# Performance work log

Measured on AMD Instinct MI355X. Metric: run time of the kernel, lower is better.

## Reference

```python
import jax, jax.numpy as jnp
import numpy as np

N = 50000
E = 1600000
IN_DIM = 128
H = 8
D = 16  # out_dim per head


def setup_inputs() -> dict:
    key = jax.random.key(0)
    ks = jax.random.split(key, 9)
    h = jax.random.normal(ks[0], (N, IN_DIM), dtype=jnp.float32)
    src = jax.random.randint(ks[1], (E,), 0, N, dtype=jnp.int32)
    dst = jax.random.randint(ks[2], (E,), 0, N, dtype=jnp.int32)
    s = 1.0 / np.sqrt(IN_DIM)
    WQ = jax.random.uniform(ks[3], (IN_DIM, H * D), jnp.float32, -s, s)
    WK = jax.random.uniform(ks[4], (IN_DIM, H * D), jnp.float32, -s, s)
    WV = jax.random.uniform(ks[5], (IN_DIM, H * D), jnp.float32, -s, s)
    bQ = jax.random.uniform(ks[6], (H * D,), jnp.float32, -s, s)
    bK = jax.random.uniform(ks[7], (H * D,), jnp.float32, -s, s)
    bV = jax.random.uniform(ks[8], (H * D,), jnp.float32, -s, s)
    return {"h": h, "src": src, "dst": dst, "WQ": WQ, "WK": WK, "WV": WV,
            "bQ": bQ, "bK": bK, "bV": bV}


def reference(h, src, dst, WQ, WK, WV, bQ, bK, bV):
    # Node projections -> [N, H, D]
    Q = (h @ WQ + bQ).reshape(-1, H, D)
    K = (h @ WK + bK).reshape(-1, H, D)
    V = (h @ WV + bV).reshape(-1, H, D)
    # Edge scores: dot(K[src], Q[dst]) per head, scaled+clamped exp -> [E, H]
    scale = jnp.float32(np.sqrt(D))
    score = jnp.exp(jnp.clip(jnp.sum(K[src] * Q[dst], axis=-1) / scale, -5.0, 5.0))
    # Scatter-sum to destination nodes
    wV = jax.ops.segment_sum(score[:, :, None] * V[src], dst, num_segments=N)  # [N, H, D]
    z = jax.ops.segment_sum(score, dst, num_segments=N)  # [N, H]
    return wV / z[:, :, None]
```

## Files before the change

kernel.cpp:

```cpp
#include <hip/hip_runtime.h>

#define N_NODES 50000
#define N_PAD   50048
#define N_EDGES 1600000
#define HD 128
#define CHUNK 4096
#define NCHUNK ((N_EDGES + CHUNK - 1) / CHUNK)
#define NBUCKET ((N_NODES + 127) / 128)
#define PROJ_BLOCKS (N_PAD / 64)

typedef __attribute__((ext_vector_type(8))) short short8;
typedef __attribute__((ext_vector_type(4))) float floatx4;
typedef __attribute__((ext_vector_type(2))) float float2v;

union U4S8 { uint4 u; short8 s; };

__device__ __forceinline__ unsigned short f2bf(float f) {
    unsigned u = __float_as_uint(f);
    unsigned r = (u + 0x7fffu + ((u >> 16) & 1u)) >> 16;
    return (unsigned short)r;
}

__global__ __launch_bounds__(256) void k_chunkhist(
    const int* __restrict__ dst, int* __restrict__ chunkhist, int* __restrict__ btot,
    const float* __restrict__ WQ, const float* __restrict__ WK, const float* __restrict__ WV,
    unsigned short* __restrict__ Wf) {
    int t = threadIdx.x, c = blockIdx.x;
    if (c >= NCHUNK) {
        int tid = (c - NCHUNK) * 256 + t;
        int lane = tid & 63;
        int kstep = (tid >> 6) & 3;
        int ntile = tid >> 8;
        int g = ntile >> 3;
        int col = (ntile & 7) * 16 + (lane & 15);
        int k0 = kstep * 32 + (lane >> 4) * 8;
        const float* W = (g == 0) ? WQ : (g == 1) ? WK : WV;
        unsigned short r[8];
#pragma unroll
        for (int j = 0; j < 8; ++j)
            r[j] = f2bf(W[(size_t)(k0 + j) * HD + col]);
        *(uint4*)(Wf + (size_t)tid * 8) = *(uint4*)r;
        return;
    }
    __shared__ int hist[NBUCKET];
    for (int i = t; i < NBUCKET; i += 256) hist[i] = 0;
    __syncthreads();
    int e0 = c * CHUNK;
    int cnt = min(CHUNK, N_EDGES - e0);
    const uint4* d4 = (const uint4*)(dst + e0);
    int cnt4 = cnt >> 2;
    for (int i = t; i < cnt4; i += 256) {
        uint4 v = d4[i];
        atomicAdd(&hist[v.x >> 7], 1);
        atomicAdd(&hist[v.y >> 7], 1);
        atomicAdd(&hist[v.z >> 7], 1);
        atomicAdd(&hist[v.w >> 7], 1);
    }
    __syncthreads();
    for (int i = t; i < NBUCKET; i += 256) {
        int v = hist[i];
        chunkhist[c * NBUCKET + i] = v;
        if (v) atomicAdd(&btot[i], v);
    }
}

__global__ __launch_bounds__(256) void k_choff(const int* __restrict__ chunkhist,
                                               const int* __restrict__ btot,
                                               int* __restrict__ bucket_ptr,
                                               int* __restrict__ chunkoff) {
    int b = blockIdx.x, t = threadIdx.x;
    int x = 0;
    for (int i = t; i < NBUCKET; i += 256)
        if (i < b) x += btot[i];
    __shared__ int red[256];
    red[t] = x;
    __syncthreads();
    for (int off = 128; off > 0; off >>= 1) {
        if (t < off) red[t] += red[t + off];
        __syncthreads();
    }
    int base = red[0];
    if (t == 0) {
        bucket_ptr[b] = base;
        if (b == NBUCKET - 1) bucket_ptr[NBUCKET] = base + btot[b];
    }
    const int PER = (NCHUNK + 255) / 256;
    int c0 = t * PER;
    int v[PER];
    int s = 0;
#pragma unroll
    for (int i = 0; i < PER; ++i) {
        int c = c0 + i;
        v[i] = (c < NCHUNK) ? chunkhist[c * NBUCKET + b] : 0;
        s += v[i];
    }
    __shared__ int part[256];
    part[t] = s;
    __syncthreads();
    for (int off = 1; off < 256; off <<= 1) {
        int y = (t >= off) ? part[t - off] : 0;
        __syncthreads();
        part[t] += y;
        __syncthreads();
    }
    int run = base + part[t] - s;
#pragma unroll
    for (int i = 0; i < PER; ++i) {
        int c = c0 + i;
        if (c < NCHUNK) { chunkoff[c * NBUCKET + b] = run; run += v[i]; }
    }
}

__global__ __launch_bounds__(256) void k_scatter_proj(
    const int* __restrict__ src, const int* __restrict__ dst,
    const int* __restrict__ chunkoff, int* __restrict__ packed,
    const float* __restrict__ h, const unsigned short* __restrict__ Wf,
    const float* __restrict__ bQ, const float* __restrict__ bK, const float* __restrict__ bV,
    float* __restrict__ Qo, unsigned short* __restrict__ KV) {
    int c = blockIdx.x;
    int t = threadIdx.x;
    if (c >= NCHUNK) {
        int blk = c - NCHUNK;
        int w = t >> 6;
        int l = t & 63;
        int row0 = blk * 64 + w * 16;
        int arow = row0 + (l & 15);
        int akoff = (l >> 4) * 8;
        bool rowok = arow < N_NODES;

        short8 a[4];
#pragma unroll
        for (int ks = 0; ks < 4; ++ks) {
            unsigned short r[8];
            if (rowok) {
                const float4* ap = (const float4*)(h + (size_t)arow * HD + ks * 32 + akoff);
                float4 f0 = ap[0], f1 = ap[1];
                r[0] = f2bf(f0.x); r[1] = f2bf(f0.y); r[2] = f2bf(f0.z); r[3] = f2bf(f0.w);
                r[4] = f2bf(f1.x); r[5] = f2bf(f1.y); r[6] = f2bf(f1.z); r[7] = f2bf(f1.w);
            } else {
#pragma unroll
                for (int j = 0; j < 8; ++j) r[j] = 0;
            }
            a[ks] = *(short8*)r;
        }

        int orow0 = row0 + (l >> 4) * 4;
#pragma unroll
        for (int nt = 0; nt < 24; ++nt) {
            floatx4 acc = (floatx4){0.f, 0.f, 0.f, 0.f};
#pragma unroll
            for (int ks = 0; ks < 4; ++ks) {
                U4S8 u;
                u.u = *(const uint4*)(Wf + ((size_t)(nt * 4 + ks) * 64 + l) * 8);
                acc = __builtin_amdgcn_mfma_f32_16x16x32_bf16(a[ks], u.s, acc, 0, 0, 0);
            }
            int g = nt >> 3;
            int cc = (nt & 7) * 16 + (l & 15);
            float bias = (g == 0) ? bQ[cc] : (g == 1) ? bK[cc] : bV[cc];
            int headoff = (cc >> 4) * 32 + (cc & 15);
#pragma unroll
            for (int r = 0; r < 4; ++r) {
                int grow = orow0 + r;
                if (grow < N_NODES) {
                    float val = acc[r] + bias;
                    if (g == 0)      Qo[(size_t)grow * HD + cc] = val;
                    else if (g == 1) KV[(size_t)grow * 256 + headoff] = f2bf(val);
                    else             KV[(size_t)grow * 256 + headoff + 16] = f2bf(val);
                }
            }
        }
        return;
    }
    __shared__ int cur[NBUCKET];
    for (int i = t; i < NBUCKET; i += 256) cur[i] = chunkoff[c * NBUCKET + i];
    __syncthreads();
    int e0 = c * CHUNK;
    int cnt = min(CHUNK, N_EDGES - e0);
    const uint4* d4 = (const uint4*)(dst + e0);
    const uint4* s4 = (const uint4*)(src + e0);
    int cnt4 = cnt >> 2;
    for (int i = t; i < cnt4; i += 256) {
        uint4 d = d4[i];
        uint4 s = s4[i];
        int pos;
        pos = atomicAdd(&cur[d.x >> 7], 1); packed[pos] = (s.x << 7) | (d.x & 127);
        pos = atomicAdd(&cur[d.y >> 7], 1); packed[pos] = (s.y << 7) | (d.y & 127);
        pos = atomicAdd(&cur[d.z >> 7], 1); packed[pos] = (s.z << 7) | (d.z & 127);
        pos = atomicAdd(&cur[d.w >> 7], 1); packed[pos] = (s.w << 7) | (d.w & 127);
    }
}

__global__ __launch_bounds__(256) void k_finalize(const int* __restrict__ bucket_ptr,
                                                  const int* __restrict__ packed,
                                                  int* __restrict__ row_ptr,
                                                  int* __restrict__ col_src) {
    __shared__ int hist[128], part[128], cur[128];
    int b = blockIdx.x, t = threadIdx.x;
    if (t < 128) hist[t] = 0;
    __syncthreads();
    int ebeg = bucket_ptr[b], eend = bucket_ptr[b + 1];
    int m = eend - ebeg;
    for (int i = t; i < m; i += 256)
        atomicAdd(&hist[packed[ebeg + i] & 127], 1);
    __syncthreads();
    int v = 0;
    if (t < 128) { v = hist[t]; part[t] = v; }
    __syncthreads();
    for (int off = 1; off < 128; off <<= 1) {
        int x = 0;
        if (t < 128 && t >= off) x = part[t - off];
        __syncthreads();
        if (t < 128) part[t] += x;
        __syncthreads();
    }
    if (t < 128) {
        int excl = part[t] - v;
        int node = b * 128 + t;
        if (node < N_NODES) row_ptr[node] = ebeg + excl;
        if (node == N_NODES - 1) row_ptr[N_NODES] = eend;
        cur[t] = ebeg + excl;
    }
    __syncthreads();
    for (int i = t; i < m; i += 256) {
        int p = packed[ebeg + i];
        int pos = atomicAdd(&cur[p & 127], 1);
        col_src[pos] = p >> 7;
    }
}


__device__ __forceinline__ float2v bf2f2(unsigned u) {
    float2v r;
    r.x = __uint_as_float(u << 16);
    r.y = __uint_as_float(u & 0xffff0000u);
    return r;
}
#define FMA2(a, b, c) __builtin_elementwise_fma((a), (b), (c))

#define LOADKV(K0, K1, V0, V1, blk)                                        \
    {                                                                      \
        int _b = (blk) < smax ? (blk) : smax;                              \
        int _s = __shfl(e_l, 8 * _b + o);                                  \
        const uint4* _kv = (const uint4*)(KVp + (size_t)_s * 256);         \
        K0 = _kv[0]; K1 = _kv[1]; V0 = _kv[2]; V1 = _kv[3];                \
    }

#define STEPC(K0, K1, V0, V1, blk)                                         \
    {                                                                      \
        float2v d2 = FMA2(bf2f2(K0.x), qp0, Z2);                           \
        d2 = FMA2(bf2f2(K0.y), qp1, d2);                                   \
        d2 = FMA2(bf2f2(K0.z), qp2, d2);                                   \
        d2 = FMA2(bf2f2(K0.w), qp3, d2);                                   \
        d2 = FMA2(bf2f2(K1.x), qp4, d2);                                   \
        d2 = FMA2(bf2f2(K1.y), qp5, d2);                                   \
        d2 = FMA2(bf2f2(K1.z), qp6, d2);                                   \
        d2 = FMA2(bf2f2(K1.w), qp7, d2);                                   \
        float dot = d2.x + d2.y;                                           \
        float sc = __expf(fminf(fmaxf(dot * 0.25f, -5.f), 5.f));           \
        if (8 * (blk) + o >= mm) sc = 0.f;                                 \
        float2v sc2;                                                       \
        sc2.x = sc; sc2.y = sc;                                            \
        ac0 = FMA2(sc2, bf2f2(V0.x), ac0);                                 \
        ac1 = FMA2(sc2, bf2f2(V0.y), ac1);                                 \
        ac2 = FMA2(sc2, bf2f2(V0.z), ac2);                                 \
        ac3 = FMA2(sc2, bf2f2(V0.w), ac3);                                 \
        ac4 = FMA2(sc2, bf2f2(V1.x), ac4);                                 \
        ac5 = FMA2(sc2, bf2f2(V1.y), ac5);                                 \
        ac6 = FMA2(sc2, bf2f2(V1.z), ac6);                                 \
        ac7 = FMA2(sc2, bf2f2(V1.w), ac7);                                 \
        z += sc;                                                           \
    }

__global__ __launch_bounds__(256) void attn_kernel(
    const float* __restrict__ Q,
    const unsigned short* __restrict__ KV,
    const int* __restrict__ row_ptr, const int* __restrict__ col_src,
    float* __restrict__ out) {
    int n = blockIdx.x * 4 + (threadIdx.x >> 6);
    if (n >= N_NODES) return;
    int l = threadIdx.x & 63;
    int o = l >> 3;
    int p = l & 7;

    const unsigned short* KVp = KV + p * 32;

    float2v Z2;
    Z2.x = 0.f; Z2.y = 0.f;

    const float4* Qv = (const float4*)(Q + (size_t)n * HD + p * 16);
    float4 q0 = Qv[0], q1 = Qv[1], q2 = Qv[2], q3 = Qv[3];
    float2v qp0, qp1, qp2, qp3, qp4, qp5, qp6, qp7;
    qp0.x = q0.x; qp0.y = q0.y;  qp1.x = q0.z; qp1.y = q0.w;
    qp2.x = q1.x; qp2.y = q1.y;  qp3.x = q1.z; qp3.y = q1.w;
    qp4.x = q2.x; qp4.y = q2.y;  qp5.x = q2.z; qp5.y = q2.w;
    qp6.x = q3.x; qp6.y = q3.y;  qp7.x = q3.z; qp7.y = q3.w;

    float2v ac0 = Z2, ac1 = Z2, ac2 = Z2, ac3 = Z2;
    float2v ac4 = Z2, ac5 = Z2, ac6 = Z2, ac7 = Z2;
    float z = 0.f;

    int beg = row_ptr[n], end = row_ptr[n + 1];

    for (int base = beg; base < end; base += 64) {
        int mm = min(64, end - base);
        int e_l = col_src[(base + l < end) ? (base + l) : beg];
        int steps = (mm + 7) >> 3;
        int smax = steps - 1;

        uint4 xK0, xK1, xV0, xV1;
        uint4 yK0, yK1, yV0, yV1;
        uint4 zK0, zK1, zV0, zV1;

        LOADKV(xK0, xK1, xV0, xV1, 0);
        LOADKV(yK0, yK1, yV0, yV1, 1);
        LOADKV(zK0, zK1, zV0, zV1, 2);

        int i = 0;
        while (true) {
            STEPC(xK0, xK1, xV0, xV1, i);
            LOADKV(xK0, xK1, xV0, xV1, i + 3);
            if (i + 1 >= steps) break;
            STEPC(yK0, yK1, yV0, yV1, i + 1);
            LOADKV(yK0, yK1, yV0, yV1, i + 4);
            if (i + 2 >= steps) break;
            STEPC(zK0, zK1, zV0, zV1, i + 2);
            LOADKV(zK0, zK1, zV0, zV1, i + 5);
            i += 3;
            if (i >= steps) break;
        }
    }

#pragma unroll
    for (int j = 0; j < 8; ++j) {
        float2v* a = (j == 0) ? &ac0 : (j == 1) ? &ac1 : (j == 2) ? &ac2 :
                     (j == 3) ? &ac3 : (j == 4) ? &ac4 : (j == 5) ? &ac5 :
                     (j == 6) ? &ac6 : &ac7;
        a->x += __shfl_xor(a->x, 8);
        a->x += __shfl_xor(a->x, 16);
        a->x += __shfl_xor(a->x, 32);
        a->y += __shfl_xor(a->y, 8);
        a->y += __shfl_xor(a->y, 16);
        a->y += __shfl_xor(a->y, 32);
    }
    z += __shfl_xor(z, 8);
    z += __shfl_xor(z, 16);
    z += __shfl_xor(z, 32);

    if (o == 0) {
        float inv = 1.f / z;
        float4* O = (float4*)(out + (size_t)n * HD + p * 16);
        O[0] = (float4){ac0.x * inv, ac0.y * inv, ac1.x * inv, ac1.y * inv};
        O[1] = (float4){ac2.x * inv, ac2.y * inv, ac3.x * inv, ac3.y * inv};
        O[2] = (float4){ac4.x * inv, ac4.y * inv, ac5.x * inv, ac5.y * inv};
        O[3] = (float4){ac6.x * inv, ac6.y * inv, ac7.x * inv, ac7.y * inv};
    }
}


static inline char* align256(char* p) {
    return (char*)(((uintptr_t)p + 255) & ~(uintptr_t)255);
}

extern "C" void kernel_launch(void* const* d_in, const int* in_sizes, int n_in,
                              void* d_out, int out_size, void* d_ws, size_t ws_size,
                              hipStream_t stream) {
    const float* h  = (const float*)d_in[0];
    const int*   src = (const int*)d_in[1];
    const int*   dst = (const int*)d_in[2];
    const float* WQ = (const float*)d_in[3];
    const float* WK = (const float*)d_in[4];
    const float* WV = (const float*)d_in[5];
    const float* bQ = (const float*)d_in[6];
    const float* bK = (const float*)d_in[7];
    const float* bV = (const float*)d_in[8];
    float* out = (float*)d_out;

    char* p = (char*)d_ws;
    float* Q = (float*)p;                    p += (size_t)N_PAD * HD * 4;
    unsigned short* KV = (unsigned short*)p; p += (size_t)N_PAD * 256 * 2;
    unsigned short* Wf = (unsigned short*)p; p += (size_t)24 * 4 * 64 * 8 * 2;
    p = align256(p);
    int* row_ptr    = (int*)p;               p += (N_NODES + 2) * 4;
    p = align256(p);
    int* bucket_ptr = (int*)p;               p += (NBUCKET + 1) * 4;
    p = align256(p);
    int* btot       = (int*)p;               p += NBUCKET * 4;
    p = align256(p);
    int* chunkhist  = (int*)p;               p += (size_t)NCHUNK * NBUCKET * 4;
    p = align256(p);
    int* chunkoff   = (int*)p;               p += (size_t)NCHUNK * NBUCKET * 4;
    p = align256(p);
    int* packed     = (int*)p;               p += (size_t)N_EDGES * 4;
    p = align256(p);
    int* col_src    = (int*)p;               p += (size_t)N_EDGES * 4;

    (void)hipMemsetAsync(btot, 0, NBUCKET * sizeof(int), stream);
    k_chunkhist<<<NCHUNK + 24, 256, 0, stream>>>(dst, chunkhist, btot, WQ, WK, WV, Wf);
    k_choff<<<NBUCKET, 256, 0, stream>>>(chunkhist, btot, bucket_ptr, chunkoff);
    k_scatter_proj<<<NCHUNK + PROJ_BLOCKS, 256, 0, stream>>>(
        src, dst, chunkoff, packed, h, Wf, bQ, bK, bV, Q, KV);
    k_finalize<<<NBUCKET, 256, 0, stream>>>(bucket_ptr, packed, row_ptr, col_src);
    attn_kernel<<<(N_NODES + 3) / 4, 256, 0, stream>>>(Q, KV, row_ptr, col_src, out);
}
```

Baseline: 271.2 us.

## Replace two-level bucketed CSR build with direct global-atomic counting sort

Replaces the chunked bucket histogram, per-chunk offset scan, packed scatter and per-bucket finalize with a flat per-node global atomic histogram, a block-wise prefix scan, and a direct global-atomic scatter of src into col_src. This drops one kernel launch, the packed intermediate array and the chunk-offset tables. In exchange it does 3.2M global atomics on node counters instead of LDS atomics. The scan recomputes each block's prefix by summing all earlier counts, which is quadratic-ish work. Edge order within each row becomes nondeterministic, which the old scheme also allowed.

```diff
diff --git a/kernel.cpp b/kernel.cpp
--- a/kernel.cpp
+++ b/kernel.cpp
@@ -4,9 +4,10 @@
 #define N_PAD   50048
 #define N_EDGES 1600000
 #define HD 128
-#define CHUNK 4096
-#define NCHUNK ((N_EDGES + CHUNK - 1) / CHUNK)
-#define NBUCKET ((N_NODES + 127) / 128)
+#define EDGE4 (N_EDGES / 4)
+#define HISTB ((EDGE4 + 255) / 256)
+#define SCANB 196
+#define NSCAN (SCANB * 256)
 #define PROJ_BLOCKS (N_PAD / 64)
 
 typedef __attribute__((ext_vector_type(8))) short short8;
@@ -21,13 +22,13 @@
     return (unsigned short)r;
 }
 
-__global__ __launch_bounds__(256) void k_chunkhist(
-    const int* __restrict__ dst, int* __restrict__ chunkhist, int* __restrict__ btot,
+__global__ __launch_bounds__(256) void k_hist(
+    const int* __restrict__ dst, int* __restrict__ cnt,
     const float* __restrict__ WQ, const float* __restrict__ WK, const float* __restrict__ WV,
     unsigned short* __restrict__ Wf) {
     int t = threadIdx.x, c = blockIdx.x;
-    if (c >= NCHUNK) {
-        int tid = (c - NCHUNK) * 256 + t;
+    if (c >= HISTB) {
+        int tid = (c - HISTB) * 256 + t;
         int lane = tid & 63;
         int kstep = (tid >> 6) & 3;
         int ntile = tid >> 8;
@@ -42,36 +43,22 @@
         *(uint4*)(Wf + (size_t)tid * 8) = *(uint4*)r;
         return;
     }
-    __shared__ int hist[NBUCKET];
-    for (int i = t; i < NBUCKET; i += 256) hist[i] = 0;
-    __syncthreads();
-    int e0 = c * CHUNK;
-    int cnt = min(CHUNK, N_EDGES - e0);
-    const uint4* d4 = (const uint4*)(dst + e0);
-    int cnt4 = cnt >> 2;
-    for (int i = t; i < cnt4; i += 256) {
-        uint4 v = d4[i];
-        atomicAdd(&hist[v.x >> 7], 1);
-        atomicAdd(&hist[v.y >> 7], 1);
-        atomicAdd(&hist[v.z >> 7], 1);
-        atomicAdd(&hist[v.w >> 7], 1);
-    }
-    __syncthreads();
-    for (int i = t; i < NBUCKET; i += 256) {
-        int v = hist[i];
-        chunkhist[c * NBUCKET + i] = v;
-        if (v) atomicAdd(&btot[i], v);
-    }
-}
-
-__global__ __launch_bounds__(256) void k_choff(const int* __restrict__ chunkhist,
-                                               const int* __restrict__ btot,
-                                               int* __restrict__ bucket_ptr,
-                                               int* __restrict__ chunkoff) {
+    int i = c * 256 + t;
+    if (i < EDGE4) {
+        uint4 d = ((const uint4*)dst)[i];
+        atomicAdd(&cnt[d.x], 1);
+        atomicAdd(&cnt[d.y], 1);
+        atomicAdd(&cnt[d.z], 1);
+        atomicAdd(&cnt[d.w], 1);
+    }
+}
+
+__global__ __launch_bounds__(256) void k_scan(const int* __restrict__ cnt,
+                                              int* __restrict__ row_ptr,
+                                              int* __restrict__ cur) {
     int b = blockIdx.x, t = threadIdx.x;
     int x = 0;
-    for (int i = t; i < NBUCKET; i += 256)
-        if (i < b) x += btot[i];
+    for (int i = t; i < b * 256; i += 256) x += cnt[i];
     __shared__ int red[256];
     red[t] = x;
     __syncthreads();
@@ -80,22 +67,11 @@
         __syncthreads();
     }
     int base = red[0];
-    if (t == 0) {
-        bucket_ptr[b] = base;
-        if (b == NBUCKET - 1) bucket_ptr[NBUCKET] = base + btot[b];
-    }
-    const int PER = (NCHUNK + 255) / 256;
-    int c0 = t * PER;
-    int v[PER];
-    int s = 0;
-#pragma unroll
-    for (int i = 0; i < PER; ++i) {
-        int c = c0 + i;
-        v[i] = (c < NCHUNK) ? chunkhist[c * NBUCKET + b] : 0;
-        s += v[i];
-    }
+    __syncthreads();
+    int node = b * 256 + t;
+    int v = (node < N_NODES) ? cnt[node] : 0;
     __shared__ int part[256];
-    part[t] = s;
+    part[t] = v;
     __syncthreads();
     for (int off = 1; off < 256; off <<= 1) {
         int y = (t >= off) ? part[t - off] : 0;
@@ -103,24 +79,22 @@
         part[t] += y;
         __syncthreads();
     }
-    int run = base + part[t] - s;
-#pragma unroll
-    for (int i = 0; i < PER; ++i) {
-        int c = c0 + i;
-        if (c < NCHUNK) { chunkoff[c * NBUCKET + b] = run; run += v[i]; }
-    }
+    int excl = base + part[t] - v;
+    if (node < N_NODES) row_ptr[node] = excl;
+    if (node == N_NODES - 1) row_ptr[N_NODES] = excl + v;
+    if (node < NSCAN) cur[node] = excl;
 }
 
 __global__ __launch_bounds__(256) void k_scatter_proj(
     const int* __restrict__ src, const int* __restrict__ dst,
-    const int* __restrict__ chunkoff, int* __restrict__ packed,
+    int* __restrict__ cur, int* __restrict__ col_src,
     const float* __restrict__ h, const unsigned short* __restrict__ Wf,
     const float* __restrict__ bQ, const float* __restrict__ bK, const float* __restrict__ bV,
     float* __restrict__ Qo, unsigned short* __restrict__ KV) {
     int c = blockIdx.x;
     int t = threadIdx.x;
-    if (c >= NCHUNK) {
-        int blk = c - NCHUNK;
+    if (c >= HISTB) {
+        int blk = c - HISTB;
         int w = t >> 6;
         int l = t & 63;
         int row0 = blk * 64 + w * 16;
@@ -171,60 +145,15 @@
         }
         return;
     }
-    __shared__ int cur[NBUCKET];
-    for (int i = t; i < NBUCKET; i += 256) cur[i] = chunkoff[c * NBUCKET + i];
-    __syncthreads();
-    int e0 = c * CHUNK;
-    int cnt = min(CHUNK, N_EDGES - e0);
-    const uint4* d4 = (const uint4*)(dst + e0);
-    const uint4* s4 = (const uint4*)(src + e0);
-    int cnt4 = cnt >> 2;
-    for (int i = t; i < cnt4; i += 256) {
-        uint4 d = d4[i];
-        uint4 s = s4[i];
+    int i = c * 256 + t;
+    if (i < EDGE4) {
+        uint4 d = ((const uint4*)dst)[i];
+        uint4 s = ((const uint4*)src)[i];
         int pos;
-        pos = atomicAdd(&cur[d.x >> 7], 1); packed[pos] = (s.x << 7) | (d.x & 127);
-        pos = atomicAdd(&cur[d.y >> 7], 1); packed[pos] = (s.y << 7) | (d.y & 127);
-        pos = atomicAdd(&cur[d.z >> 7], 1); packed[pos] = (s.z << 7) | (d.z & 127);
-        pos = atomicAdd(&cur[d.w >> 7], 1); packed[pos] = (s.w << 7) | (d.w & 127);
-    }
-}
-
-__global__ __launch_bounds__(256) void k_finalize(const int* __restrict__ bucket_ptr,
-                                                  const int* __restrict__ packed,
-                                                  int* __restrict__ row_ptr,
-                                                  int* __restrict__ col_src) {
-    __shared__ int hist[128], part[128], cur[128];
-    int b = blockIdx.x, t = threadIdx.x;
-    if (t < 128) hist[t] = 0;
-    __syncthreads();
-    int ebeg = bucket_ptr[b], eend = bucket_ptr[b + 1];
-    int m = eend - ebeg;
-    for (int i = t; i < m; i += 256)
-        atomicAdd(&hist[packed[ebeg + i] & 127], 1);
-    __syncthreads();
-    int v = 0;
-    if (t < 128) { v = hist[t]; part[t] = v; }
-    __syncthreads();
-    for (int off = 1; off < 128; off <<= 1) {
-        int x = 0;
-        if (t < 128 && t >= off) x = part[t - off];
-        __syncthreads();
-        if (t < 128) part[t] += x;
-        __syncthreads();
-    }
-    if (t < 128) {
-        int excl = part[t] - v;
-        int node = b * 128 + t;
-        if (node < N_NODES) row_ptr[node] = ebeg + excl;
-        if (node == N_NODES - 1) row_ptr[N_NODES] = eend;
-        cur[t] = ebeg + excl;
-    }
-    __syncthreads();
-    for (int i = t; i < m; i += 256) {
-        int p = packed[ebeg + i];
-        int pos = atomicAdd(&cur[p & 127], 1);
-        col_src[pos] = p >> 7;
+        pos = atomicAdd(&cur[d.x], 1); col_src[pos] = s.x;
+        pos = atomicAdd(&cur[d.y], 1); col_src[pos] = s.y;
+        pos = atomicAdd(&cur[d.z], 1); col_src[pos] = s.z;
+        pos = atomicAdd(&cur[d.w], 1); col_src[pos] = s.w;
     }
 }
 
@@ -380,25 +309,18 @@
     unsigned short* KV = (unsigned short*)p; p += (size_t)N_PAD * 256 * 2;
     unsigned short* Wf = (unsigned short*)p; p += (size_t)24 * 4 * 64 * 8 * 2;
     p = align256(p);
-    int* row_ptr    = (int*)p;               p += (N_NODES + 2) * 4;
+    int* row_ptr = (int*)p;                  p += (N_NODES + 2) * 4;
     p = align256(p);
-    int* bucket_ptr = (int*)p;               p += (NBUCKET + 1) * 4;
+    int* cnt     = (int*)p;                  p += NSCAN * 4;
     p = align256(p);
-    int* btot       = (int*)p;               p += NBUCKET * 4;
+    int* cur     = (int*)p;                  p += NSCAN * 4;
     p = align256(p);
-    int* chunkhist  = (int*)p;               p += (size_t)NCHUNK * NBUCKET * 4;
-    p = align256(p);
-    int* chunkoff   = (int*)p;               p += (size_t)NCHUNK * NBUCKET * 4;
-    p = align256(p);
-    int* packed     = (int*)p;               p += (size_t)N_EDGES * 4;
-    p = align256(p);
-    int* col_src    = (int*)p;               p += (size_t)N_EDGES * 4;
-
-    (void)hipMemsetAsync(btot, 0, NBUCKET * sizeof(int), stream);
-    k_chunkhist<<<NCHUNK + 24, 256, 0, stream>>>(dst, chunkhist, btot, WQ, WK, WV, Wf);
-    k_choff<<<NBUCKET, 256, 0, stream>>>(chunkhist, btot, bucket_ptr, chunkoff);
-    k_scatter_proj<<<NCHUNK + PROJ_BLOCKS, 256, 0, stream>>>(
-        src, dst, chunkoff, packed, h, Wf, bQ, bK, bV, Q, KV);
-    k_finalize<<<NBUCKET, 256, 0, stream>>>(bucket_ptr, packed, row_ptr, col_src);
+    int* col_src = (int*)p;                  p += (size_t)N_EDGES * 4;
+
+    (void)hipMemsetAsync(cnt, 0, NSCAN * sizeof(int), stream);
+    k_hist<<<HISTB + 24, 256, 0, stream>>>(dst, cnt, WQ, WK, WV, Wf);
+    k_scan<<<SCANB, 256, 0, stream>>>(cnt, row_ptr, cur);
+    k_scatter_proj<<<HISTB + PROJ_BLOCKS, 256, 0, stream>>>(
+        src, dst, cur, col_src, h, Wf, bQ, bK, bV, Q, KV);
     attn_kernel<<<(N_NODES + 3) / 4, 256, 0, stream>>>(Q, KV, row_ptr, col_src, out);
 }
```

New measurement: 439.3 us. 62.0% more time.

## Stage K/V gathers through LDS with async global_load_lds double buffering

Applied to the files above, without the earlier changes.

Replaces the register-held, three-deep K/V prefetch with direct global-to-LDS async loads into a per-wave double buffer. Manual s_waitcnt vmcnt guards each step, and each lane then reads its K/V slice back from LDS. The aim is to free the many VGPRs held by the prefetch registers and let the load path bypass registers. In exchange, prefetch depth drops from three steps ahead to one, an LDS round trip is added, and the early return for out-of-range nodes is removed.

```diff
diff --git a/kernel.cpp b/kernel.cpp
--- a/kernel.cpp
+++ b/kernel.cpp
@@ -237,12 +237,24 @@
 }
 #define FMA2(a, b, c) __builtin_elementwise_fma((a), (b), (c))
 
-#define LOADKV(K0, K1, V0, V1, blk)                                        \
-    {                                                                      \
-        int _b = (blk) < smax ? (blk) : smax;                              \
-        int _s = __shfl(e_l, 8 * _b + o);                                  \
-        const uint4* _kv = (const uint4*)(KVp + (size_t)_s * 256);         \
-        K0 = _kv[0]; K1 = _kv[1]; V0 = _kv[2]; V1 = _kv[3];                \
+#define ISSUE(blk, par)                                                     \
+    {                                                                       \
+        int _b = (blk) < smax ? (blk) : smax;                               \
+        int _s = __shfl(e_l, 8 * _b + o);                                   \
+        const char* _g = KVb + ((size_t)_s << 9) + (p << 6);                \
+        char* _l = (char*)&stage[w][par][0];                                \
+        __builtin_amdgcn_global_load_lds(                                   \
+            (const __attribute__((address_space(1))) void*)(_g),            \
+            (__attribute__((address_space(3))) void*)(_l), 16, 0, 0);       \
+        __builtin_amdgcn_global_load_lds(                                   \
+            (const __attribute__((address_space(1))) void*)(_g + 16),       \
+            (__attribute__((address_space(3))) void*)(_l + 1024), 16, 0, 0);\
+        __builtin_amdgcn_global_load_lds(                                   \
+            (const __attribute__((address_space(1))) void*)(_g + 32),       \
+            (__attribute__((address_space(3))) void*)(_l + 2048), 16, 0, 0);\
+        __builtin_amdgcn_global_load_lds(                                   \
+            (const __attribute__((address_space(1))) void*)(_g + 48),       \
+            (__attribute__((address_space(3))) void*)(_l + 3072), 16, 0, 0);\
     }
 
 #define STEPC(K0, K1, V0, V1, blk)                                         \
@@ -276,13 +288,14 @@
     const unsigned short* __restrict__ KV,
     const int* __restrict__ row_ptr, const int* __restrict__ col_src,
     float* __restrict__ out) {
+    __shared__ uint4 stage[4][2][256];
     int n = blockIdx.x * 4 + (threadIdx.x >> 6);
-    if (n >= N_NODES) return;
+    int w = threadIdx.x >> 6;
     int l = threadIdx.x & 63;
     int o = l >> 3;
     int p = l & 7;
 
-    const unsigned short* KVp = KV + p * 32;
+    const char* KVb = (const char*)KV;
 
     float2v Z2;
     Z2.x = 0.f; Z2.y = 0.f;
@@ -307,26 +320,21 @@
         int steps = (mm + 7) >> 3;
         int smax = steps - 1;
 
-        uint4 xK0, xK1, xV0, xV1;
-        uint4 yK0, yK1, yV0, yV1;
-        uint4 zK0, zK1, zV0, zV1;
-
-        LOADKV(xK0, xK1, xV0, xV1, 0);
-        LOADKV(yK0, yK1, yV0, yV1, 1);
-        LOADKV(zK0, zK1, zV0, zV1, 2);
-
-        int i = 0;
-        while (true) {
-            STEPC(xK0, xK1, xV0, xV1, i);
-            LOADKV(xK0, xK1, xV0, xV1, i + 3);
-            if (i + 1 >= steps) break;
-            STEPC(yK0, yK1, yV0, yV1, i + 1);
-            LOADKV(yK0, yK1, yV0, yV1, i + 4);
-            if (i + 2 >= steps) break;
-            STEPC(zK0, zK1, zV0, zV1, i + 2);
-            LOADKV(zK0, zK1, zV0, zV1, i + 5);
-            i += 3;
-            if (i >= steps) break;
+        ISSUE(0, 0);
+        for (int i = 0; i < steps; ++i) {
+            int par = i & 1;
+            if (i + 1 < steps) {
+                ISSUE(i + 1, par ^ 1);
+                asm volatile("s_waitcnt vmcnt(4)" ::: "memory");
+            } else {
+                asm volatile("s_waitcnt vmcnt(0)" ::: "memory");
+            }
+            const uint4* sb = &stage[w][par][0];
+            uint4 K0 = sb[l];
+            uint4 K1 = sb[64 + l];
+            uint4 V0 = sb[128 + l];
+            uint4 V1 = sb[192 + l];
+            STEPC(K0, K1, V0, V1, i);
         }
     }
 
```

New measurement: 266.7 us. No clear change (-1.7%).
